# Optimization experiments

Measured on AMD Instinct MI355X. Metric: run time of the kernel, lower is better.

The kernel has to match this reference:

```python
import jax, jax.numpy as jnp
import numpy as np

B, IN, HID = 8192, 2048, 2048


def setup_inputs() -> dict:
    key = jax.random.key(0)
    ks = jax.random.split(key, 8)
    s_in = 1.0 / np.sqrt(IN + HID)  # torch Linear default init scale (uniform bound)
    inp = {
        "x": jax.random.normal(ks[0], (B, IN), jnp.float32),
        "h_prev": jax.random.normal(ks[1], (B, HID), jnp.float32),
        "c_prev": jax.random.normal(ks[2], (B, HID), jnp.float32),
        "embedding_vec": jnp.zeros((B, 1), jnp.float32),  # ignored in vanilla mode
        "Wf": jax.random.normal(ks[3], (IN + HID, HID), jnp.float32) * s_in,
        "Wi": jax.random.normal(ks[4], (IN + HID, HID), jnp.float32) * s_in,
        "Wc": jax.random.normal(ks[5], (IN + HID, HID), jnp.float32) * s_in,
        "Wo": jax.random.normal(ks[6], (IN + HID, HID), jnp.float32) * s_in,
        "bf": jnp.zeros((HID,), jnp.float32),
        "bi": jnp.zeros((HID,), jnp.float32),
        "bc": jnp.zeros((HID,), jnp.float32),
        "bo": jnp.zeros((HID,), jnp.float32),
    }
    return inp


def reference(x, h_prev, c_prev, embedding_vec, Wf, Wi, Wc, Wo, bf, bi, bc, bo):
    # rearrange_inputs: concat flattened x with h_prev; embedding_vec ignored
    cat = jnp.concatenate([x.reshape(x.shape[0], -1), h_prev], axis=1)  # [B, IN+HID]
    # Fuse the four gate GEMMs into one: [B, IN+HID] @ [IN+HID, 4*HID]
    W = jnp.concatenate([Wf, Wi, Wc, Wo], axis=1)
    b = jnp.concatenate([bf, bi, bc, bo], axis=0)
    z = cat @ W + b  # [B, 4*HID]
    zf, zi, zc, zo = jnp.split(z, 4, axis=1)
    f_t = jax.nn.sigmoid(zf)
    i_t = jax.nn.sigmoid(zi)
    c_opt = jnp.tanh(zc)
    c_t = c_prev * f_t + i_t * c_opt
    o_t = jax.nn.sigmoid(zo)
    h_t = o_t * jnp.tanh(c_t)
    return (h_t, c_t)
```

## Files before the change

kernel.cpp:

```cpp
#include <hip/hip_runtime.h>
#include <stdint.h>

#define B_SZ   8192
#define IN_SZ  2048
#define HIDN   2048
#define KTOT   4096
#define BKk    32
#define NKS    (KTOT / BKk)
#define GRID_F 1024

typedef __attribute__((ext_vector_type(8))) short short8;
typedef __attribute__((ext_vector_type(8))) unsigned short ushort8;
typedef __attribute__((ext_vector_type(4))) float float4v;

static __device__ __forceinline__ float bf2f(uint16_t h) {
  union { uint32_t u; float f; } v; v.u = ((uint32_t)h) << 16; return v.f;
}
static __device__ __forceinline__ uint16_t f2bf(float f) {
  union { float f; uint32_t u; } v; v.f = f;
  uint32_t r = v.u + 0x7FFFu + ((v.u >> 16) & 1u);
  return (uint16_t)(r >> 16);
}
static __device__ __forceinline__ float sigmoidf_(float v) {
  return 1.f / (1.f + __expf(-v));
}
static __device__ __forceinline__ float tanhf_(float v) {
  return 1.f - 2.f / (1.f + __expf(2.f * v));
}

static __device__ __forceinline__ ushort8 load8(const void* base, size_t eidx, int isf32) {
  ushort8 r;
  if (isf32) {
    const float* p = (const float*)base + eidx;
    float4v a = *(const float4v*)p;
    float4v b = *(const float4v*)(p + 4);
    r[0] = f2bf(a[0]); r[1] = f2bf(a[1]); r[2] = f2bf(a[2]); r[3] = f2bf(a[3]);
    r[4] = f2bf(b[0]); r[5] = f2bf(b[1]); r[6] = f2bf(b[2]); r[7] = f2bf(b[3]);
  } else {
    r = *(const ushort8*)((const uint16_t*)base + eidx);
  }
  return r;
}

static __device__ __forceinline__ void gll16(const void* g, void* l) {
  __builtin_amdgcn_global_load_lds(
      (const __attribute__((address_space(1))) uint32_t*)g,
      (__attribute__((address_space(3))) uint32_t*)l, 16, 0, 0);
}

static __device__ __forceinline__ void bar() {
  asm volatile("" ::: "memory");
  __builtin_amdgcn_s_barrier();
  asm volatile("" ::: "memory");
}

__global__ __launch_bounds__(64) void detect_kernel(const uint32_t* __restrict__ x,
                                                    int* __restrict__ flag) {
  const int lane = threadIdx.x;
  int cnt = 0;
  #pragma unroll
  for (int s = 0; s < 8; ++s) {
    uint32_t u = x[lane + s * 64];
    int e = (u >> 7) & 0xFF;
    int hit = (e >= 117 && e <= 131) ? 1 : 0;
    cnt += (int)__popcll(__ballot(hit));
  }
  if (lane == 0) *flag = (cnt < 256) ? 1 : 0;
}

__global__ __launch_bounds__(256) void wtrans_kernel(
    const void* __restrict__ Wf, const void* __restrict__ Wi,
    const void* __restrict__ Wc, const void* __restrict__ Wo,
    uint16_t* __restrict__ Wt, const int* __restrict__ flagp)
{
  __shared__ uint16_t tile[4 * 64 * 128];
  const int isf32 = *flagp;
  const int k0 = blockIdx.x * 128;
  const int n0 = blockIdx.y * 64;
  const int tid = threadIdx.x;
  const void* Wg4[4] = {Wf, Wi, Wc, Wo};

  #pragma unroll
  for (int s = 0; s < 16; ++s) {
    const int flat = s * 256 + tid;
    const int g = flat >> 10;
    const int r = (flat >> 3) & 127;
    const int c = flat & 7;
    ushort8 v = load8(Wg4[g], (size_t)(k0 + r) * HIDN + n0 + c * 8, isf32);
    uint16_t* trow = tile + (g * 64 + c * 8) * 128 + (r & 7) + 8 * ((r >> 3) ^ c);
    #pragma unroll
    for (int e = 0; e < 8; ++e) trow[e * 128] = v[e];
  }
  __syncthreads();

  #pragma unroll
  for (int s = 0; s < 16; ++s) {
    const int flat = s * 256 + tid;
    const int kc = flat & 15;
    const int np = flat >> 4;
    const int n  = np >> 2;
    ushort8 v = *(const ushort8*)(tile + (np & 3) * 8192 + n * 128 +
                                  ((kc ^ (n >> 3)) * 8));
    *(ushort8*)(Wt + (size_t)(n0 * 4 + np) * KTOT + k0 + kc * 8) = v;
  }
}

__global__ __launch_bounds__(256) void catconv_kernel(
    const void* __restrict__ x, const void* __restrict__ h,
    uint16_t* __restrict__ catB, const int* __restrict__ flagp)
{
  const int isf32 = *flagp;
  const void* src = blockIdx.y ? h : x;
  const size_t t = (size_t)blockIdx.x * 256 + threadIdx.x;
  const int m  = (int)(t >> 8);
  const int k8 = (int)(t & 255) * 8;
  ushort8 v = load8(src, (size_t)m * IN_SZ + k8, isf32);
  *(ushort8*)(catB + (size_t)m * KTOT + (size_t)blockIdx.y * IN_SZ + k8) = v;
}

extern "C" __global__ __launch_bounds__(512, 2) void lstm_fused_kernel(
    const uint16_t* __restrict__ Wt, const uint16_t* __restrict__ catB,
    const void* __restrict__ cprev,
    const void* __restrict__ bfv, const void* __restrict__ biv,
    const void* __restrict__ bcv, const void* __restrict__ bov,
    void* __restrict__ outbase, const int* __restrict__ flagp)
{
  extern __shared__ __align__(16) char ldsbuf[];

  const int isf32 = *flagp;
  const int tid  = threadIdx.x;
  const int lane = tid & 63;
  const int wave = tid >> 6;
  const int l15  = lane & 15;
  const int quad = lane >> 4;
  const int wr   = wave >> 2;
  const int wc   = wave & 3;

  const int bid = blockIdx.x;
  const int xcd = bid & 7, loc = bid >> 3;
  const int nt  = xcd * 4 + (loc & 3);
  const int mt  = loc >> 2;
  const int mB  = mt * 256;
  const int nB  = nt * 256;
  const int nb4 = nt * 64;

  const int srow = lane >> 2;
  const int scol = ((lane & 3) ^ ((lane >> 3) & 3)) * 8;
  const uint16_t* aSrc[2];
  const uint16_t* bSrc[2];
  #pragma unroll
  for (int s = 0; s < 2; ++s) {
    aSrc[s] = Wt   + (size_t)(nB + (s * 8 + wave) * 16 + srow) * KTOT + scol;
    bSrc[s] = catB + (size_t)(mB + (s * 8 + wave) * 16 + srow) * KTOT + scol;
  }

  const int rswz = (quad ^ ((l15 >> 1) & 3)) << 4;
  int offA[8], offB[4];
  #pragma unroll
  for (int i = 0; i < 8; ++i)
    offA[i] = (wr * 8 + i) * 1024 + l15 * 64 + rswz;
  #pragma unroll
  for (int j = 0; j < 4; ++j)
    offB[j] = 16384 + (wc * 4 + j) * 1024 + l15 * 64 + rswz;

  float4v acc[8][4];
  #pragma unroll
  for (int i = 0; i < 8; ++i)
    #pragma unroll
    for (int j = 0; j < 4; ++j)
      acc[i][j] = {0.f, 0.f, 0.f, 0.f};

  #pragma unroll
  for (int tt = 0; tt < 3; ++tt) {
    const size_t kk = (size_t)tt * BKk;
    const int bb = (tt & 3) * 32768 + wave * 1024;
    gll16(aSrc[0] + kk, ldsbuf + bb);
    gll16(aSrc[1] + kk, ldsbuf + bb + 8192);
    gll16(bSrc[0] + kk, ldsbuf + bb + 16384);
    gll16(bSrc[1] + kk, ldsbuf + bb + 16384 + 8192);
  }
  asm volatile("s_waitcnt vmcnt(8)" ::: "memory");
  bar();

#define KSTEP(T, DO_STAGE, VMSTR)                                              \
  {                                                                            \
    const int bb = ((T) & 3) * 32768;                                          \
    short8 af[4], bfr[4];                                                      \
    _Pragma("unroll")                                                          \
    for (int j = 0; j < 4; ++j)                                                \
      bfr[j] = *(const short8*)(ldsbuf + bb + offB[j]);                        \
    _Pragma("unroll")                                                          \
    for (int ii = 0; ii < 4; ++ii)                                             \
      af[ii] = *(const short8*)(ldsbuf + bb + offA[ii]);                       \
    if (DO_STAGE) {                                                            \
      const size_t kk = (size_t)((T) + 3) * BKk;                               \
      const int sb = (((T) + 3) & 3) * 32768 + wave * 1024;                    \
      gll16(aSrc[0] + kk, ldsbuf + sb);                                        \
      gll16(aSrc[1] + kk, ldsbuf + sb + 8192);                                 \
    }                                                                          \
    bar();                                                                     \
    __builtin_amdgcn_s_setprio(1);                                             \
    _Pragma("unroll")                                                          \
    for (int ii = 0; ii < 4; ++ii)                                             \
      _Pragma("unroll")                                                        \
      for (int j = 0; j < 4; ++j)                                              \
        acc[ii][j] = __builtin_amdgcn_mfma_f32_16x16x32_bf16(                  \
            af[ii], bfr[j], acc[ii][j], 0, 0, 0);                              \
    __builtin_amdgcn_s_setprio(0);                                             \
    bar();                                                                     \
    _Pragma("unroll")                                                          \
    for (int ii = 0; ii < 4; ++ii)                                             \
      af[ii] = *(const short8*)(ldsbuf + bb + offA[4 + ii]);                   \
    if (DO_STAGE) {                                                            \
      const size_t kk = (size_t)((T) + 3) * BKk;                               \
      const int sb = (((T) + 3) & 3) * 32768 + 16384 + wave * 1024;            \
      gll16(bSrc[0] + kk, ldsbuf + sb);                                        \
      gll16(bSrc[1] + kk, ldsbuf + sb + 8192);                                 \
    }                                                                          \
    asm volatile("s_waitcnt " VMSTR ::: "memory");                             \
    bar();                                                                     \
    __builtin_amdgcn_s_setprio(1);                                             \
    _Pragma("unroll")                                                          \
    for (int ii = 0; ii < 4; ++ii)                                             \
      _Pragma("unroll")                                                        \
      for (int j = 0; j < 4; ++j)                                              \
        acc[4 + ii][j] = __builtin_amdgcn_mfma_f32_16x16x32_bf16(              \
            af[ii], bfr[j], acc[4 + ii][j], 0, 0, 0);                          \
    __builtin_amdgcn_s_setprio(0);                                             \
    bar();                                                                     \
  }

  for (int t = 0; t < NKS - 3; ++t) KSTEP(t, 1, "vmcnt(8)");
  KSTEP(NKS - 3, 0, "vmcnt(4)");
  KSTEP(NKS - 2, 0, "vmcnt(0)");
  KSTEP(NKS - 1, 0, "vmcnt(0)");
#undef KSTEP

  #pragma unroll
  for (int i = 0; i < 8; ++i) {
    const int ng = nb4 + wr * 32 + i * 4 + quad;
    const float bfx = isf32 ? ((const float*)bfv)[ng] : bf2f(((const uint16_t*)bfv)[ng]);
    const float bix = isf32 ? ((const float*)biv)[ng] : bf2f(((const uint16_t*)biv)[ng]);
    const float bcx = isf32 ? ((const float*)bcv)[ng] : bf2f(((const uint16_t*)bcv)[ng]);
    const float box = isf32 ? ((const float*)bov)[ng] : bf2f(((const uint16_t*)bov)[ng]);
    #pragma unroll
    for (int j = 0; j < 4; ++j) {
      const int mg = mB + wc * 64 + j * 16 + l15;
      float4v z = acc[i][j];
      const float ft  = sigmoidf_(z[0] + bfx);
      const float it  = sigmoidf_(z[1] + bix);
      const float cto = tanhf_(z[2] + bcx);
      const float ot  = sigmoidf_(z[3] + box);
      const float cp  = isf32 ? ((const float*)cprev)[(size_t)mg * HIDN + ng]
                              : bf2f(((const uint16_t*)cprev)[(size_t)mg * HIDN + ng]);
      const float cvv = cp * ft + it * cto;
      acc[i][j][0] = ot * tanhf_(cvv);
      acc[i][j][1] = cvv;
    }
  }

  if (!isf32) {
    uint16_t* hout = (uint16_t*)outbase;
    uint16_t* cout = hout + (size_t)B_SZ * HIDN;
    uint16_t* hb = (uint16_t*)ldsbuf;
    uint16_t* cb = (uint16_t*)(ldsbuf + 32768);
    #pragma unroll
    for (int i = 0; i < 8; ++i) {
      const int ncl = wr * 32 + i * 4 + quad;
      #pragma unroll
      for (int j = 0; j < 4; ++j) {
        const int ml = wc * 64 + j * 16 + l15;
        hb[ml * 64 + ncl] = f2bf(acc[i][j][0]);
        cb[ml * 64 + ncl] = f2bf(acc[i][j][1]);
      }
    }
    __syncthreads();
    #pragma unroll
    for (int s = 0; s < 4; ++s) {
      const int off = tid * 16 + s * 8192;
      const int row = off >> 7;
      const int c8  = (off >> 4) & 7;
      const size_t g = (size_t)(mB + row) * HIDN + nb4 + c8 * 8;
      *(ushort8*)(hout + g) = *(const ushort8*)(ldsbuf + off);
      *(ushort8*)(cout + g) = *(const ushort8*)(ldsbuf + 32768 + off);
    }
  } else {
    float* hout = (float*)outbase;
    float* cout = hout + (size_t)B_SZ * HIDN;
    float* fbH = (float*)ldsbuf;
    float* fbC = (float*)(ldsbuf + 65536);
    #pragma unroll
    for (int i = 0; i < 8; ++i) {
      const int ncl = wr * 32 + i * 4 + quad;
      #pragma unroll
      for (int j = 0; j < 4; ++j) {
        const int ml = wc * 64 + j * 16 + l15;
        fbH[ml * 64 + ncl] = acc[i][j][0];
        fbC[ml * 64 + ncl] = acc[i][j][1];
      }
    }
    __syncthreads();
    #pragma unroll
    for (int s = 0; s < 8; ++s) {
      const int off = tid * 16 + s * 8192;
      const int row = off >> 8;
      const int c4  = (off >> 4) & 15;
      const size_t g = (size_t)(mB + row) * HIDN + nb4 + c4 * 4;
      *(float4v*)(hout + g) = *(const float4v*)(ldsbuf + off);
      *(float4v*)(cout + g) = *(const float4v*)(ldsbuf + 65536 + off);
    }
  }
}

extern "C" void kernel_launch(void* const* d_in, const int* in_sizes, int n_in,
                              void* d_out, int out_size, void* d_ws, size_t ws_size,
                              hipStream_t stream) {
  const void* x   = d_in[0];
  const void* h   = d_in[1];
  const void* c   = d_in[2];
  const void* Wf  = d_in[4];
  const void* Wi  = d_in[5];
  const void* Wc  = d_in[6];
  const void* Wo  = d_in[7];
  const void* bf_ = d_in[8];
  const void* bi_ = d_in[9];
  const void* bc_ = d_in[10];
  const void* bo_ = d_in[11];

  int*      flag = (int*)d_ws;
  uint16_t* Wt   = (uint16_t*)((char*)d_ws + 256);
  uint16_t* catB = (uint16_t*)((char*)d_ws + 256 + (size_t)64 * 1024 * 1024);

  static int lds_configured = 0;
  if (!lds_configured) {
    hipFuncSetAttribute((const void*)lstm_fused_kernel,
                        hipFuncAttributeMaxDynamicSharedMemorySize, 131072);
    lds_configured = 1;
  }

  hipLaunchKernelGGL(detect_kernel, dim3(1), dim3(64), 0, stream,
                     (const uint32_t*)x, flag);
  hipLaunchKernelGGL(wtrans_kernel, dim3(KTOT / 128, HIDN / 64, 1), dim3(256), 0, stream,
                     Wf, Wi, Wc, Wo, Wt, flag);
  hipLaunchKernelGGL(catconv_kernel, dim3(B_SZ * IN_SZ / (8 * 256), 2, 1), dim3(256), 0, stream,
                     x, h, catB, flag);
  hipLaunchKernelGGL(lstm_fused_kernel, dim3(GRID_F), dim3(512), 131072, stream,
                     Wt, catB, c, bf_, bi_, bc_, bo_, d_out, flag);
}
```

Baseline: 875.7 us.

## Merge prep kernels into one launch and swizzle epilogue LDS staging

```diff
diff --git a/kernel.cpp b/kernel.cpp
--- a/kernel.cpp
+++ b/kernel.cpp
@@ -54,68 +54,71 @@
   asm volatile("" ::: "memory");
 }
 
-__global__ __launch_bounds__(64) void detect_kernel(const uint32_t* __restrict__ x,
-                                                    int* __restrict__ flag) {
-  const int lane = threadIdx.x;
+__global__ __launch_bounds__(256) void prep_kernel(
+    const void* __restrict__ x, const void* __restrict__ h,
+    const void* __restrict__ Wf, const void* __restrict__ Wi,
+    const void* __restrict__ Wc, const void* __restrict__ Wo,
+    uint16_t* __restrict__ Wt, uint16_t* __restrict__ catB,
+    int* __restrict__ flag)
+{
+  __shared__ uint16_t tile[4 * 64 * 128];
+  const int tid  = threadIdx.x;
+  const int lane = tid & 63;
+
   int cnt = 0;
   #pragma unroll
   for (int s = 0; s < 8; ++s) {
-    uint32_t u = x[lane + s * 64];
+    uint32_t u = ((const uint32_t*)x)[lane + s * 64];
     int e = (u >> 7) & 0xFF;
     int hit = (e >= 117 && e <= 131) ? 1 : 0;
     cnt += (int)__popcll(__ballot(hit));
   }
-  if (lane == 0) *flag = (cnt < 256) ? 1 : 0;
-}
-
-__global__ __launch_bounds__(256) void wtrans_kernel(
-    const void* __restrict__ Wf, const void* __restrict__ Wi,
-    const void* __restrict__ Wc, const void* __restrict__ Wo,
-    uint16_t* __restrict__ Wt, const int* __restrict__ flagp)
-{
-  __shared__ uint16_t tile[4 * 64 * 128];
-  const int isf32 = *flagp;
-  const int k0 = blockIdx.x * 128;
-  const int n0 = blockIdx.y * 64;
-  const int tid = threadIdx.x;
-  const void* Wg4[4] = {Wf, Wi, Wc, Wo};
-
-  #pragma unroll
-  for (int s = 0; s < 16; ++s) {
-    const int flat = s * 256 + tid;
-    const int g = flat >> 10;
-    const int r = (flat >> 3) & 127;
-    const int c = flat & 7;
-    ushort8 v = load8(Wg4[g], (size_t)(k0 + r) * HIDN + n0 + c * 8, isf32);
-    uint16_t* trow = tile + (g * 64 + c * 8) * 128 + (r & 7) + 8 * ((r >> 3) ^ c);
-    #pragma unroll
-    for (int e = 0; e < 8; ++e) trow[e * 128] = v[e];
-  }
-  __syncthreads();
-
-  #pragma unroll
-  for (int s = 0; s < 16; ++s) {
-    const int flat = s * 256 + tid;
-    const int kc = flat & 15;
-    const int np = flat >> 4;
-    const int n  = np >> 2;
-    ushort8 v = *(const ushort8*)(tile + (np & 3) * 8192 + n * 128 +
-                                  ((kc ^ (n >> 3)) * 8));
-    *(ushort8*)(Wt + (size_t)(n0 * 4 + np) * KTOT + k0 + kc * 8) = v;
-  }
-}
-
-__global__ __launch_bounds__(256) void catconv_kernel(
-    const void* __restrict__ x, const void* __restrict__ h,
-    uint16_t* __restrict__ catB, const int* __restrict__ flagp)
-{
-  const int isf32 = *flagp;
-  const void* src = blockIdx.y ? h : x;
-  const size_t t = (size_t)blockIdx.x * 256 + threadIdx.x;
-  const int m  = (int)(t >> 8);
-  const int k8 = (int)(t & 255) * 8;
-  ushort8 v = load8(src, (size_t)m * IN_SZ + k8, isf32);
-  *(ushort8*)(catB + (size_t)m * KTOT + (size_t)blockIdx.y * IN_SZ + k8) = v;
+  const int isf32 = (cnt < 256) ? 1 : 0;
+
+  const int bid = blockIdx.x;
+  if (bid == 0 && tid == 0) *flag = isf32;
+
+  const int q = bid / 5, r5 = bid % 5;
+  if (r5 == 0) {
+    const int k0 = (q & 31) * 128;
+    const int n0 = (q >> 5) * 64;
+    const void* Wg4[4] = {Wf, Wi, Wc, Wo};
+
+    #pragma unroll
+    for (int s = 0; s < 16; ++s) {
+      const int flat = s * 256 + tid;
+      const int g = flat >> 10;
+      const int r = (flat >> 3) & 127;
+      const int c = flat & 7;
+      ushort8 v = load8(Wg4[g], (size_t)(k0 + r) * HIDN + n0 + c * 8, isf32);
+      uint16_t* trow = tile + (g * 64 + c * 8) * 128 + (r & 7) + 8 * ((r >> 3) ^ c);
+      #pragma unroll
+      for (int e = 0; e < 8; ++e) trow[e * 128] = v[e];
+    }
+    __syncthreads();
+
+    #pragma unroll
+    for (int s = 0; s < 16; ++s) {
+      const int flat = s * 256 + tid;
+      const int kc = flat & 15;
+      const int np = flat >> 4;
+      const int n  = np >> 2;
+      ushort8 v = *(const ushort8*)(tile + (np & 3) * 8192 + n * 128 +
+                                    ((kc ^ (n >> 3)) * 8));
+      *(ushort8*)(Wt + (size_t)(n0 * 4 + np) * KTOT + k0 + kc * 8) = v;
+    }
+  } else {
+    const int c    = bid - q - 1;
+    const int half = c >> 11;
+    const void* src = half ? h : x;
+    const int row  = (c & 2047) * 4 + (tid >> 6);
+    #pragma unroll
+    for (int s = 0; s < 4; ++s) {
+      const int col = lane * 8 + s * 512;
+      ushort8 v = load8(src, (size_t)row * IN_SZ + col, isf32);
+      *(ushort8*)(catB + (size_t)row * KTOT + half * IN_SZ + col) = v;
+    }
+  }
 }
 
 extern "C" __global__ __launch_bounds__(512, 2) void lstm_fused_kernel(
@@ -269,9 +272,10 @@
       const int ncl = wr * 32 + i * 4 + quad;
       #pragma unroll
       for (int j = 0; j < 4; ++j) {
-        const int ml = wc * 64 + j * 16 + l15;
-        hb[ml * 64 + ncl] = f2bf(acc[i][j][0]);
-        cb[ml * 64 + ncl] = f2bf(acc[i][j][1]);
+        const int ml  = wc * 64 + j * 16 + l15;
+        const int nph = (ncl & 7) | ((((ncl >> 3) ^ (ml & 7)) & 7) << 3);
+        hb[ml * 64 + nph] = f2bf(acc[i][j][0]);
+        cb[ml * 64 + nph] = f2bf(acc[i][j][1]);
       }
     }
     __syncthreads();
@@ -280,9 +284,10 @@
       const int off = tid * 16 + s * 8192;
       const int row = off >> 7;
       const int c8  = (off >> 4) & 7;
+      const int bo  = row * 128 + ((c8 ^ (row & 7)) * 16);
       const size_t g = (size_t)(mB + row) * HIDN + nb4 + c8 * 8;
-      *(ushort8*)(hout + g) = *(const ushort8*)(ldsbuf + off);
-      *(ushort8*)(cout + g) = *(const ushort8*)(ldsbuf + 32768 + off);
+      *(ushort8*)(hout + g) = *(const ushort8*)(ldsbuf + bo);
+      *(ushort8*)(cout + g) = *(const ushort8*)(ldsbuf + 32768 + bo);
     }
   } else {
     float* hout = (float*)outbase;
@@ -294,9 +299,10 @@
       const int ncl = wr * 32 + i * 4 + quad;
       #pragma unroll
       for (int j = 0; j < 4; ++j) {
-        const int ml = wc * 64 + j * 16 + l15;
-        fbH[ml * 64 + ncl] = acc[i][j][0];
-        fbC[ml * 64 + ncl] = acc[i][j][1];
+        const int ml  = wc * 64 + j * 16 + l15;
+        const int nph = (ncl & 3) | ((((ncl >> 2) ^ (ml & 15)) & 15) << 2);
+        fbH[ml * 64 + nph] = acc[i][j][0];
+        fbC[ml * 64 + nph] = acc[i][j][1];
       }
     }
     __syncthreads();
@@ -305,9 +311,10 @@
       const int off = tid * 16 + s * 8192;
       const int row = off >> 8;
       const int c4  = (off >> 4) & 15;
+      const int bo  = row * 256 + ((c4 ^ (row & 15)) * 16);
       const size_t g = (size_t)(mB + row) * HIDN + nb4 + c4 * 4;
-      *(float4v*)(hout + g) = *(const float4v*)(ldsbuf + off);
-      *(float4v*)(cout + g) = *(const float4v*)(ldsbuf + 65536 + off);
+      *(float4v*)(hout + g) = *(const float4v*)(ldsbuf + bo);
+      *(float4v*)(cout + g) = *(const float4v*)(ldsbuf + 65536 + bo);
     }
   }
 }
@@ -338,12 +345,8 @@
     lds_configured = 1;
   }
 
-  hipLaunchKernelGGL(detect_kernel, dim3(1), dim3(64), 0, stream,
-                     (const uint32_t*)x, flag);
-  hipLaunchKernelGGL(wtrans_kernel, dim3(KTOT / 128, HIDN / 64, 1), dim3(256), 0, stream,
-                     Wf, Wi, Wc, Wo, Wt, flag);
-  hipLaunchKernelGGL(catconv_kernel, dim3(B_SZ * IN_SZ / (8 * 256), 2, 1), dim3(256), 0, stream,
-                     x, h, catB, flag);
+  hipLaunchKernelGGL(prep_kernel, dim3(5120), dim3(256), 0, stream,
+                     x, h, Wf, Wi, Wc, Wo, Wt, catB, flag);
   hipLaunchKernelGGL(lstm_fused_kernel, dim3(GRID_F), dim3(512), 131072, stream,
                      Wt, catB, c, bf_, bi_, bc_, bo_, d_out, flag);
 }
```

Result: no change. 874.2 us (-0.2%).
